# Kernel optimization log

Measured on AMD Instinct MI355X. Metric: run time of the kernel, lower is better.

The kernel has to match this reference:

```python
import jax, jax.numpy as jnp
import numpy as np

B, L, V, S = 256, 20, 9488, 18  # batch, decode length, vocab (Mp1), target seq_length


def setup_inputs() -> dict:
    key = jax.random.key(0)
    k1, k2, k3, k4 = jax.random.split(key, 4)
    # per-timestep log-probabilities over the vocabulary
    inp = jax.random.normal(k1, (B, L, V), dtype=jnp.float32)
    # ground-truth word indices; 0 is the pad/EOS token
    target = jax.random.randint(k2, (B, S), 0, V)
    # scalar CIDEr rewards (computed on CPU in the original; plain floats here)
    reward = jax.random.uniform(k3, (1,), dtype=jnp.float32)
    reward1 = jax.random.uniform(k4, (1,), dtype=jnp.float32)
    return {"input": inp, "target": target, "reward": reward, "reward1": reward1}


def reference(input, target, reward, reward1):
    b, l, v = input.shape
    s = target.shape[1]
    t_len = l - 1  # loop runs t = 1 .. L-1, reading target[:, t-1]
    # extend target with zeros for positions t-1 >= seq_length, truncate to L-1
    pad = max(t_len - s, 0)
    tgt = jnp.concatenate(
        [target, jnp.zeros((b, pad), dtype=target.dtype)], axis=1
    )[:, :t_len]  # [B, L-1]
    # include every token up to and INCLUDING the first zero; break at second zero
    # => position kept iff inclusive cumulative zero-count <= 1
    is_zero = (tgt == 0)
    mask = (jnp.cumsum(is_zero, axis=1) <= 1).astype(input.dtype)  # [B, L-1]
    # gather log-prob of the target word at each kept position
    logp = jnp.take_along_axis(input[:, 1:, :], tgt[..., None], axis=2)[..., 0]  # [B, L-1]
    n = jnp.sum(mask)
    reward_diff = jnp.maximum(reward[0] - reward1[0], jnp.asarray(1.0, input.dtype))
    loss = -(jnp.sum(logp * mask) / n) * reward_diff
    return loss
```

## Files before the change

kernel.cpp:

```cpp
#include <hip/hip_runtime.h>

constexpr int kB = 256;
constexpr int kL = 20;
constexpr int kV = 9488;
constexpr int kS = 18;
constexpr int kT = kL - 1;

__global__ __launch_bounds__(256) void scst_loss_kernel(
    const float* __restrict__ inp,
    const int* __restrict__ target,
    const float* __restrict__ reward,
    const float* __restrict__ reward1,
    float* __restrict__ out)
{
    __shared__ int tgt_lds[kB * kS];
    const int tid = threadIdx.x;

    #pragma unroll
    for (int i = 0; i < kS; ++i) {
        const int idx = i * kB + tid;
        tgt_lds[idx] = target[idx];
    }
    __syncthreads();

    const int b = tid;
    const float* row = inp + (size_t)b * kL * kV + kV;

    float sum = 0.0f;
    int cnt = 0;
    int zc = 0;
    #pragma unroll
    for (int t = 0; t < kT; ++t) {
        const int w = (t < kS) ? tgt_lds[b * kS + t] : 0;
        zc += (w == 0) ? 1 : 0;
        if (zc <= 1) {
            sum += row[(size_t)t * kV + w];
            cnt += 1;
        }
    }

    #pragma unroll
    for (int off = 32; off >= 1; off >>= 1) {
        sum += __shfl_down(sum, off, 64);
        cnt += __shfl_down(cnt, off, 64);
    }

    __shared__ float wsum[4];
    __shared__ int   wcnt[4];
    const int wave = tid >> 6;
    const int lane = tid & 63;
    if (lane == 0) { wsum[wave] = sum; wcnt[wave] = cnt; }
    __syncthreads();

    if (tid == 0) {
        const float s = wsum[0] + wsum[1] + wsum[2] + wsum[3];
        const int   c = wcnt[0] + wcnt[1] + wcnt[2] + wcnt[3];
        float rd = reward[0] - reward1[0];
        rd = (rd > 1.0f) ? rd : 1.0f;
        out[0] = -(s / (float)c) * rd;
    }
}

extern "C" void kernel_launch(void* const* d_in, const int* in_sizes, int n_in,
                              void* d_out, int out_size, void* d_ws, size_t ws_size,
                              hipStream_t stream) {
    const float* inp     = (const float*)d_in[0];
    const int*   target  = (const int*)d_in[1];
    const float* reward  = (const float*)d_in[2];
    const float* reward1 = (const float*)d_in[3];
    float* out = (float*)d_out;

    scst_loss_kernel<<<1, 256, 0, stream>>>(inp, target, reward, reward1, out);
}
```

Before: 232.7 us.

## Split gather-reduce across timestep blocks with a second finalize kernel

Replaces the single-block kernel with one block per timestep, so the 19 dependent random gathers per thread are spread over 19 blocks and issued in parallel. Each block recomputes the zero-count prefix for its timestep, reduces a sum and count, and writes a float2 partial to the workspace. A second one-wave kernel sums the partials and applies the reward scaling. This adds a second kernel launch and redundant loads of the target array into LDS in every block, in exchange for much more memory-level parallelism.

```diff
diff --git a/kernel.cpp b/kernel.cpp
--- a/kernel.cpp
+++ b/kernel.cpp
@@ -6,58 +6,72 @@
 constexpr int kS = 18;
 constexpr int kT = kL - 1;
 
-__global__ __launch_bounds__(256) void scst_loss_kernel(
+__global__ __launch_bounds__(256) void scst_partial_kernel(
     const float* __restrict__ inp,
     const int* __restrict__ target,
+    float2* __restrict__ partials)
+{
+    __shared__ int tgt_lds[kB * kS];
+    const int b = threadIdx.x;
+    const int t = blockIdx.x;
+
+    #pragma unroll
+    for (int i = 0; i < kS; ++i) {
+        const int idx = i * kB + b;
+        tgt_lds[idx] = target[idx];
+    }
+    __syncthreads();
+
+    const int w = (t < kS) ? tgt_lds[b * kS + t] : 0;
+    const float val = inp[(size_t)b * kL * kV + (size_t)(t + 1) * kV + w];
+
+    int zc = (t >= kS) ? 1 : 0;
+    const int imax = (t < kS) ? t : (kS - 1);
+    for (int i = 0; i <= imax; ++i)
+        zc += (tgt_lds[b * kS + i] == 0) ? 1 : 0;
+
+    const bool m = (zc <= 1);
+    float s = m ? val : 0.0f;
+    int   c = m ? 1 : 0;
+
+    #pragma unroll
+    for (int off = 32; off >= 1; off >>= 1) {
+        s += __shfl_down(s, off, 64);
+        c += __shfl_down(c, off, 64);
+    }
+    __shared__ float wsum[4];
+    __shared__ int   wcnt[4];
+    const int wave = b >> 6;
+    const int lane = b & 63;
+    if (lane == 0) { wsum[wave] = s; wcnt[wave] = c; }
+    __syncthreads();
+    if (b == 0) {
+        partials[t] = make_float2(wsum[0] + wsum[1] + wsum[2] + wsum[3],
+                                  (float)(wcnt[0] + wcnt[1] + wcnt[2] + wcnt[3]));
+    }
+}
+
+__global__ __launch_bounds__(64) void scst_final_kernel(
+    const float2* __restrict__ partials,
     const float* __restrict__ reward,
     const float* __restrict__ reward1,
     float* __restrict__ out)
 {
-    __shared__ int tgt_lds[kB * kS];
-    const int tid = threadIdx.x;
-
-    #pragma unroll
-    for (int i = 0; i < kS; ++i) {
-        const int idx = i * kB + tid;
-        tgt_lds[idx] = target[idx];
+    const int lane = threadIdx.x;
+    float s = 0.0f, c = 0.0f;
+    if (lane < kT) {
+        const float2 p = partials[lane];
+        s = p.x; c = p.y;
     }
-    __syncthreads();
-
-    const int b = tid;
-    const float* row = inp + (size_t)b * kL * kV + kV;
-
-    float sum = 0.0f;
-    int cnt = 0;
-    int zc = 0;
-    #pragma unroll
-    for (int t = 0; t < kT; ++t) {
-        const int w = (t < kS) ? tgt_lds[b * kS + t] : 0;
-        zc += (w == 0) ? 1 : 0;
-        if (zc <= 1) {
-            sum += row[(size_t)t * kV + w];
-            cnt += 1;
-        }
-    }
-
     #pragma unroll
     for (int off = 32; off >= 1; off >>= 1) {
-        sum += __shfl_down(sum, off, 64);
-        cnt += __shfl_down(cnt, off, 64);
+        s += __shfl_down(s, off, 64);
+        c += __shfl_down(c, off, 64);
     }
-
-    __shared__ float wsum[4];
-    __shared__ int   wcnt[4];
-    const int wave = tid >> 6;
-    const int lane = tid & 63;
-    if (lane == 0) { wsum[wave] = sum; wcnt[wave] = cnt; }
-    __syncthreads();
-
-    if (tid == 0) {
-        const float s = wsum[0] + wsum[1] + wsum[2] + wsum[3];
-        const int   c = wcnt[0] + wcnt[1] + wcnt[2] + wcnt[3];
+    if (lane == 0) {
         float rd = reward[0] - reward1[0];
         rd = (rd > 1.0f) ? rd : 1.0f;
-        out[0] = -(s / (float)c) * rd;
+        out[0] = -(s / c) * rd;
     }
 }
 
@@ -69,6 +83,8 @@
     const float* reward  = (const float*)d_in[2];
     const float* reward1 = (const float*)d_in[3];
     float* out = (float*)d_out;
+    float2* partials = (float2*)d_ws;
 
-    scst_loss_kernel<<<1, 256, 0, stream>>>(inp, target, reward, reward1, out);
+    scst_partial_kernel<<<kT, 256, 0, stream>>>(inp, target, partials);
+    scst_final_kernel<<<1, 64, 0, stream>>>(partials, reward, reward1, out);
 }
```

New measurement: 224.0 us. 1.04x faster.
